# Optimization experiments

Hardware: AMD Instinct MI355X
Metric: run time of the kernel (lower is better)

The kernel has to match this reference:

```python
import jax, jax.numpy as jnp
import numpy as np

NUM_USER = 50000
NUM_ITEM = 40000
N = NUM_USER + NUM_ITEM
E_HALF = 500000
DIM = 64
NUM_ROUTING = 3
NEG_SLOPE = 0.01


def setup_inputs() -> dict:
    key = jax.random.key(0)
    ks = jax.random.split(key, 10)
    rng = np.random.default_rng(0)
    u = rng.integers(0, NUM_USER, E_HALF)
    it = rng.integers(NUM_USER, N, E_HALF)
    edge_index = jnp.asarray(
        np.stack([np.concatenate([u, it]), np.concatenate([it, u])]), dtype=jnp.int64
    )  # [2, 1M] bidirected user-item edges
    return {
        "edge_index": edge_index,
        "v_feat": jax.random.normal(ks[0], (NUM_ITEM, 2048), jnp.float32),
        "t_feat": jax.random.normal(ks[1], (NUM_ITEM, 384), jnp.float32),
        "pref_v": jax.random.normal(ks[2], (NUM_USER, DIM), jnp.float32),
        "pref_t": jax.random.normal(ks[3], (NUM_USER, DIM), jnp.float32),
        "W_v": jax.random.normal(ks[4], (2048, DIM), jnp.float32) * 0.02,
        "b_v": jnp.zeros((DIM,), jnp.float32),
        "W_t": jax.random.normal(ks[5], (384, DIM), jnp.float32) * 0.05,
        "b_t": jnp.zeros((DIM,), jnp.float32),
        "id_embedding": jax.random.normal(ks[6], (N, DIM), jnp.float32),
        "conf": jax.random.normal(ks[7], (N, 2), jnp.float32),
    }


def l2norm(x, eps=1e-12):
    n = jnp.sqrt(jnp.sum(x * x, axis=1, keepdims=True))
    return x / jnp.maximum(n, eps)


def leaky_relu(x):
    return jnp.where(x >= 0, x, NEG_SLOPE * x)


def segment_softmax(logits, seg, n):
    m = jax.ops.segment_max(logits, seg, num_segments=n)
    m = jnp.where(jnp.isfinite(m), m, 0.0)  # empty segments
    e = jnp.exp(logits - jax.lax.stop_gradient(m)[seg])
    s = jax.ops.segment_sum(e, seg, num_segments=n)
    return e / (s[seg] + 1e-16)


def gat_conv(x, ei):
    # dot-product attention, segment softmax over targets, scatter-add
    src, dst = ei[0], ei[1]
    xj = x[src]  # [E, D]
    alpha = jnp.sum(x[dst] * xj, axis=-1)  # [E]
    alpha = segment_softmax(alpha, dst, x.shape[0])
    out = jax.ops.segment_sum(xj * alpha[:, None], dst, num_segments=x.shape[0])
    return out, alpha


def sage_mean(x, ei, w):
    src, dst = ei[0], ei[1]
    msg = x[src] * w  # [E, D]
    s = jax.ops.segment_sum(msg, dst, num_segments=x.shape[0])
    cnt = jax.ops.segment_sum(jnp.ones((ei.shape[1],), x.dtype), dst, num_segments=x.shape[0])
    return s / jnp.maximum(cnt, 1.0)[:, None]


def cgcn(feat, pref, W, b, ei):
    features = l2norm(leaky_relu(feat @ W + b))  # [num_item, D]
    pref = l2norm(pref)
    for _ in range(NUM_ROUTING):
        x = jnp.concatenate([pref, features], axis=0)
        xh, _ = gat_conv(x, ei)
        pref = l2norm(pref + xh[:NUM_USER])
    x = jnp.concatenate([pref, features], axis=0)
    ei2 = jnp.concatenate([ei, ei[::-1]], axis=1)  # add reversed edges
    xh, alpha = gat_conv(x, ei2)
    return x + leaky_relu(xh), alpha[:, None]


def egcn(id_emb, ei, w):
    ei2 = jnp.concatenate([ei, ei[::-1]], axis=1)
    x = l2norm(id_emb)
    h1 = leaky_relu(sage_mean(x, ei2, w))
    h2 = leaky_relu(sage_mean(h1, ei2, w))
    return x + h1 + h2


def reference(edge_index, v_feat, t_feat, pref_v, pref_t, W_v, b_v, W_t, b_t,
              id_embedding, conf):
    v_rep, weight_v = cgcn(v_feat, pref_v, W_v, b_v, edge_index)
    t_rep, weight_t = cgcn(t_feat, pref_t, W_t, b_t, edge_index)
    content_rep = jnp.concatenate([v_rep, t_rep], axis=1)  # [N, 2D]
    weight = jnp.concatenate([weight_v, weight_t], axis=1)  # [2E, 2]
    # weight_mode == 'confid'
    confidence = jnp.concatenate([conf[edge_index[0]], conf[edge_index[1]]], axis=0)
    weight = jnp.max(weight * confidence, axis=1, keepdims=True)
    weight = jax.nn.relu(weight)  # pruning
    id_rep = egcn(id_embedding, edge_index, weight)
    return jnp.concatenate([id_rep, content_rep], axis=1)  # [N, 3D]
```

## Files before the change

kernel.cpp:

```cpp
#include <hip/hip_runtime.h>
#include <hip/hip_bf16.h>
#include <cstdint>
#include <cstddef>

#define NUSER 50000
#define NITEM 40000
#define NNODE 90000
#define NE    1000000
#define DIM   64

typedef __attribute__((ext_vector_type(8))) short short8;
typedef __attribute__((ext_vector_type(4))) float f32x4;

constexpr size_t O_XV   = 0;
constexpr size_t O_XT   = 5760000;
constexpr size_t O_X0   = 11520000;
constexpr size_t O_EV   = 17280000;
constexpr size_t O_ET   = 18280000;
constexpr size_t O_WE   = 19280000;
constexpr size_t O_SV   = 20280000;
constexpr size_t O_STT  = 20370000;
constexpr size_t O_DEG  = 20460000;
constexpr size_t O_RP   = 20550000;
constexpr size_t O_FILL = 20650000;
constexpr size_t O_SRC  = 20750000;
constexpr size_t O_BSUM = 21750000;
constexpr size_t O_BOFF = 21751000;
constexpr size_t O_H1   = 0;
constexpr size_t SW_VHI = 0;
constexpr size_t SW_VLO = 131072;
constexpr size_t SW_THI = 262144;
constexpr size_t SW_TLO = 286720;

__device__ __forceinline__ float leaky(float x) { return x >= 0.f ? x : 0.01f * x; }

__device__ __forceinline__ short f2bf(float x) {
  __hip_bfloat16 h = __float2bfloat16(x);
  return *reinterpret_cast<short*>(&h);
}
__device__ __forceinline__ float bf2f(short s) {
  __hip_bfloat16 h;
  *reinterpret_cast<short*>(&h) = s;
  return __bfloat162float(h);
}

__global__ void deg_count_kernel(const int* __restrict__ ei, int* __restrict__ deg) {
  int e = blockIdx.x * 256 + threadIdx.x;
  if (e >= NE) return;
  atomicAdd(&deg[ei[NE + e]], 1);
}

__global__ void block_sum_kernel(const int* __restrict__ deg, int* __restrict__ bsum) {
  __shared__ int sd[4];
  int i = blockIdx.x * 256 + threadIdx.x;
  int v = (i < NNODE) ? deg[i] : 0;
#pragma unroll
  for (int off = 32; off > 0; off >>= 1) v += __shfl_xor(v, off, 64);
  if ((threadIdx.x & 63) == 0) sd[threadIdx.x >> 6] = v;
  __syncthreads();
  if (threadIdx.x == 0) bsum[blockIdx.x] = sd[0] + sd[1] + sd[2] + sd[3];
}

__global__ void scan_bsum_kernel(const int* __restrict__ bsum, int* __restrict__ boff, int nb) {
  __shared__ int s[512];
  int t = threadIdx.x;
  int v = (t < nb) ? bsum[t] : 0;
  s[t] = v;
  __syncthreads();
  for (int off = 1; off < 512; off <<= 1) {
    int x = (t >= off) ? s[t - off] : 0;
    __syncthreads();
    s[t] += x;
    __syncthreads();
  }
  if (t < nb) boff[t] = s[t] - v;
}

__global__ void scan_final_kernel(const int* __restrict__ deg, const int* __restrict__ boff,
                                  int* __restrict__ row_ptr, int* __restrict__ fill) {
  __shared__ int s[256];
  int t = threadIdx.x;
  int i = blockIdx.x * 256 + t;
  int v = (i < NNODE) ? deg[i] : 0;
  s[t] = v;
  __syncthreads();
  for (int off = 1; off < 256; off <<= 1) {
    int x = (t >= off) ? s[t - off] : 0;
    __syncthreads();
    s[t] += x;
    __syncthreads();
  }
  int incl = s[t];
  int base = boff[blockIdx.x];
  if (i < NNODE) {
    row_ptr[i] = base + incl - v;
    fill[i] = base + incl - v;
    if (i == NNODE - 1) row_ptr[NNODE] = base + incl;
  }
}

__global__ void csr_fill_kernel(const int* __restrict__ ei, int* __restrict__ fill,
                                int* __restrict__ srcs) {
  int e = blockIdx.x * 256 + threadIdx.x;
  if (e >= NE) return;
  int s = ei[e], d = ei[NE + e];
  int slot = atomicAdd(&fill[d], 1);
  srcs[slot] = s;
}

__global__ void wsplit_kernel(const float* __restrict__ W, short* __restrict__ hi,
                              short* __restrict__ lo, int nelem) {
  int t = blockIdx.x * 256 + threadIdx.x;
  if (t >= nelem) return;
  int j = t & 7, sl = (t >> 3) & 15, q = (t >> 7) & 3, nt = (t >> 9) & 3, kt = t >> 11;
  int k = kt * 32 + q * 8 + j, n = nt * 16 + sl;
  float x = W[k * 64 + n];
  short h = f2bf(x);
  hi[t] = h;
  lo[t] = f2bf(x - bf2f(h));
}

__global__ __launch_bounds__(256) void gemm_mfma_kernel(const float* __restrict__ A,
                                                        const short* __restrict__ Whi,
                                                        const short* __restrict__ Wlo,
                                                        const float* __restrict__ bias,
                                                        float* __restrict__ out, int K) {
  __shared__ short Bsh[8192];
  __shared__ short Bsl[8192];
  int tid = threadIdx.x;
  int w = tid >> 6, lane = tid & 63, q = lane >> 4, sl = lane & 15;
  int m0 = blockIdx.x * 64;
  const float* arow = A + (size_t)(m0 + w * 16 + sl) * K;
  f32x4 acc[4] = {{0.f, 0.f, 0.f, 0.f}, {0.f, 0.f, 0.f, 0.f},
                  {0.f, 0.f, 0.f, 0.f}, {0.f, 0.f, 0.f, 0.f}};
  int nchunk = K >> 7;
  for (int c = 0; c < nchunk; ++c) {
    __syncthreads();
    const float4* srch = (const float4*)(Whi + (size_t)c * 8192);
    const float4* srcl = (const float4*)(Wlo + (size_t)c * 8192);
    float4* dsth = (float4*)Bsh;
    float4* dstl = (float4*)Bsl;
#pragma unroll
    for (int r = 0; r < 4; ++r) {
      dsth[r * 256 + tid] = srch[r * 256 + tid];
      dstl[r * 256 + tid] = srcl[r * 256 + tid];
    }
    __syncthreads();
#pragma unroll
    for (int kt = 0; kt < 4; ++kt) {
      int k = c * 128 + kt * 32 + q * 8;
      float4 a0 = *(const float4*)&arow[k];
      float4 a1 = *(const float4*)&arow[k + 4];
      float av[8] = {a0.x, a0.y, a0.z, a0.w, a1.x, a1.y, a1.z, a1.w};
      short8 ah, al;
#pragma unroll
      for (int j = 0; j < 8; ++j) {
        short h = f2bf(av[j]);
        ah[j] = h;
        al[j] = f2bf(av[j] - bf2f(h));
      }
#pragma unroll
      for (int nt = 0; nt < 4; ++nt) {
        short8 bh = *(short8*)&Bsh[(kt * 4 + nt) * 512 + lane * 8];
        short8 bl = *(short8*)&Bsl[(kt * 4 + nt) * 512 + lane * 8];
        acc[nt] = __builtin_amdgcn_mfma_f32_16x16x32_bf16(ah, bh, acc[nt], 0, 0, 0);
        acc[nt] = __builtin_amdgcn_mfma_f32_16x16x32_bf16(ah, bl, acc[nt], 0, 0, 0);
        acc[nt] = __builtin_amdgcn_mfma_f32_16x16x32_bf16(al, bh, acc[nt], 0, 0, 0);
      }
    }
  }
  float bnt[4];
#pragma unroll
  for (int nt = 0; nt < 4; ++nt) bnt[nt] = bias[nt * 16 + sl];
  float v[4][4];
#pragma unroll
  for (int nt = 0; nt < 4; ++nt)
#pragma unroll
    for (int i = 0; i < 4; ++i) v[nt][i] = leaky(acc[nt][i] + bnt[nt]);
#pragma unroll
  for (int i = 0; i < 4; ++i) {
    float ss = v[0][i] * v[0][i] + v[1][i] * v[1][i] + v[2][i] * v[2][i] + v[3][i] * v[3][i];
    ss += __shfl_xor(ss, 1);
    ss += __shfl_xor(ss, 2);
    ss += __shfl_xor(ss, 4);
    ss += __shfl_xor(ss, 8);
    float rinv = 1.f / fmaxf(sqrtf(ss), 1e-12f);
    int row = m0 + w * 16 + q * 4 + i;
#pragma unroll
    for (int nt = 0; nt < 4; ++nt)
      out[(size_t)row * 64 + nt * 16 + sl] = v[nt][i] * rinv;
  }
}

__global__ __launch_bounds__(256) void l2norm_all_kernel(const float* __restrict__ pv,
                                                         const float* __restrict__ pt,
                                                         const float* __restrict__ id,
                                                         float* __restrict__ xv,
                                                         float* __restrict__ xt,
                                                         float* __restrict__ x0) {
  int wid = (blockIdx.x * 256 + threadIdx.x) >> 6;
  int lane = threadIdx.x & 63, sub = lane >> 4, sl = lane & 15;
  int r = wid * 4 + sub;
  if (r >= 2 * NUSER + NNODE) return;
  const float* in;
  float* outp;
  int row;
  if (r < NUSER) { in = pv; outp = xv; row = r; }
  else if (r < 2 * NUSER) { in = pt; outp = xt; row = r - NUSER; }
  else { in = id; outp = x0; row = r - 2 * NUSER; }
  float4 v = *(const float4*)&in[(size_t)row * 64 + sl * 4];
  float ss = v.x * v.x + v.y * v.y + v.z * v.z + v.w * v.w;
  ss += __shfl_xor(ss, 1);
  ss += __shfl_xor(ss, 2);
  ss += __shfl_xor(ss, 4);
  ss += __shfl_xor(ss, 8);
  float rinv = 1.f / fmaxf(sqrtf(ss), 1e-12f);
  v.x *= rinv; v.y *= rinv; v.z *= rinv; v.w *= rinv;
  *(float4*)&outp[(size_t)row * 64 + sl * 4] = v;
}

__global__ __launch_bounds__(256) void routing_kernel(float* __restrict__ xv,
                                                      float* __restrict__ xt,
                                                      const int* __restrict__ rp,
                                                      const int* __restrict__ srcs) {
  int wid = (blockIdx.x * 256 + threadIdx.x) >> 6;
  int lane = threadIdx.x & 63, sub = lane >> 4, sl = lane & 15;
  if (wid >= 2 * NUSER) return;
  float* x = (wid < NUSER) ? xv : xt;
  int row = (wid < NUSER) ? wid : wid - NUSER;
  float4 p = *(const float4*)&x[(size_t)row * 64 + sl * 4];
  int jb = rp[row], je = rp[row + 1];
  float S = 0.f;
  float4 acc = {0.f, 0.f, 0.f, 0.f};
  for (int j0 = jb; j0 < je; j0 += 4) {
    int j = j0 + sub;
    bool valid = j < je;
    int jj = valid ? j : jb;
    int s = srcs[jj];
    float4 f = *(const float4*)&x[(size_t)s * 64 + sl * 4];
    float d = p.x * f.x + p.y * f.y + p.z * f.z + p.w * f.w;
    d += __shfl_xor(d, 1);
    d += __shfl_xor(d, 2);
    d += __shfl_xor(d, 4);
    d += __shfl_xor(d, 8);
    float e = valid ? __expf(d) : 0.f;
    S += e;
    acc.x += e * f.x; acc.y += e * f.y; acc.z += e * f.z; acc.w += e * f.w;
  }
  S += __shfl_xor(S, 16); S += __shfl_xor(S, 32);
  acc.x += __shfl_xor(acc.x, 16); acc.x += __shfl_xor(acc.x, 32);
  acc.y += __shfl_xor(acc.y, 16); acc.y += __shfl_xor(acc.y, 32);
  acc.z += __shfl_xor(acc.z, 16); acc.z += __shfl_xor(acc.z, 32);
  acc.w += __shfl_xor(acc.w, 16); acc.w += __shfl_xor(acc.w, 32);
  if (je > jb) {
    float r = 1.f / S;
    p.x += acc.x * r; p.y += acc.y * r; p.z += acc.z * r; p.w += acc.w * r;
  }
  float ss = p.x * p.x + p.y * p.y + p.z * p.z + p.w * p.w;
  ss += __shfl_xor(ss, 1);
  ss += __shfl_xor(ss, 2);
  ss += __shfl_xor(ss, 4);
  ss += __shfl_xor(ss, 8);
  float rinv = 1.f / fmaxf(sqrtf(ss), 1e-12f);
  if (sub == 0) {
    float4 o = {p.x * rinv, p.y * rinv, p.z * rinv, p.w * rinv};
    *(float4*)&x[(size_t)row * 64 + sl * 4] = o;
  }
}

__global__ __launch_bounds__(256) void gat_final_kernel(const float* __restrict__ xv,
                                                        const float* __restrict__ xt,
                                                        const int* __restrict__ rp,
                                                        const int* __restrict__ srcs,
                                                        float* __restrict__ eV,
                                                        float* __restrict__ eT,
                                                        float* __restrict__ SV,
                                                        float* __restrict__ ST,
                                                        float* __restrict__ out) {
  int wid = (blockIdx.x * 256 + threadIdx.x) >> 6;
  int lane = threadIdx.x & 63, sub = lane >> 4, sl = lane & 15;
  if (wid >= 2 * NNODE) return;
  const float* x;
  float* eOut;
  float* Sout;
  int row, col;
  if (wid < NNODE) { x = xv; eOut = eV; Sout = SV; row = wid; col = 64; }
  else { x = xt; eOut = eT; Sout = ST; row = wid - NNODE; col = 128; }
  float4 xn = *(const float4*)&x[(size_t)row * 64 + sl * 4];
  int jb = rp[row], je = rp[row + 1];
  float S = 0.f;
  float4 acc = {0.f, 0.f, 0.f, 0.f};
  for (int j0 = jb; j0 < je; j0 += 4) {
    int j = j0 + sub;
    bool valid = j < je;
    int jj = valid ? j : jb;
    int s = srcs[jj];
    float4 f = *(const float4*)&x[(size_t)s * 64 + sl * 4];
    float d = xn.x * f.x + xn.y * f.y + xn.z * f.z + xn.w * f.w;
    d += __shfl_xor(d, 1);
    d += __shfl_xor(d, 2);
    d += __shfl_xor(d, 4);
    d += __shfl_xor(d, 8);
    float e = valid ? __expf(d) : 0.f;
    if (valid && sl == 0) eOut[j] = e;
    S += e;
    acc.x += e * f.x; acc.y += e * f.y; acc.z += e * f.z; acc.w += e * f.w;
  }
  S += __shfl_xor(S, 16); S += __shfl_xor(S, 32);
  acc.x += __shfl_xor(acc.x, 16); acc.x += __shfl_xor(acc.x, 32);
  acc.y += __shfl_xor(acc.y, 16); acc.y += __shfl_xor(acc.y, 32);
  acc.z += __shfl_xor(acc.z, 16); acc.z += __shfl_xor(acc.z, 32);
  acc.w += __shfl_xor(acc.w, 16); acc.w += __shfl_xor(acc.w, 32);
  if (lane == 0) Sout[row] = S;
  float4 o;
  if (je > jb) {
    float r = 1.f / S;
    o.x = xn.x + leaky(acc.x * r);
    o.y = xn.y + leaky(acc.y * r);
    o.z = xn.z + leaky(acc.z * r);
    o.w = xn.w + leaky(acc.w * r);
  } else {
    o = xn;
  }
  if (sub == 0) *(float4*)&out[(size_t)row * 192 + col + sl * 4] = o;
}

__global__ __launch_bounds__(256) void egcn_h1_kernel(const float* __restrict__ x0,
                                                      const int* __restrict__ rp,
                                                      const int* __restrict__ srcs,
                                                      const float* __restrict__ eV,
                                                      const float* __restrict__ eT,
                                                      const float* __restrict__ SV,
                                                      const float* __restrict__ ST,
                                                      const float* __restrict__ conf,
                                                      float* __restrict__ wE,
                                                      float* __restrict__ h1) {
  int wid = (blockIdx.x * 256 + threadIdx.x) >> 6;
  int lane = threadIdx.x & 63, sub = lane >> 4, sl = lane & 15;
  if (wid >= NNODE) return;
  int jb = rp[wid], je = rp[wid + 1];
  float rv = 0.f, rt = 0.f;
  if (je > jb) {
    rv = 0.5f / SV[wid];
    rt = 0.5f / ST[wid];
  }
  float4 acc = {0.f, 0.f, 0.f, 0.f};
  for (int j0 = jb; j0 < je; j0 += 4) {
    int j = j0 + sub;
    bool valid = j < je;
    int jj = valid ? j : jb;
    int s = srcs[jj];
    float w = fmaxf(fmaxf(eV[jj] * rv * conf[2 * s], eT[jj] * rt * conf[2 * s + 1]), 0.f);
    if (!valid) w = 0.f;
    if (valid && sl == 0) wE[j] = w;
    float4 f = *(const float4*)&x0[(size_t)s * 64 + sl * 4];
    acc.x += f.x * w; acc.y += f.y * w; acc.z += f.z * w; acc.w += f.w * w;
  }
  acc.x += __shfl_xor(acc.x, 16); acc.x += __shfl_xor(acc.x, 32);
  acc.y += __shfl_xor(acc.y, 16); acc.y += __shfl_xor(acc.y, 32);
  acc.z += __shfl_xor(acc.z, 16); acc.z += __shfl_xor(acc.z, 32);
  acc.w += __shfl_xor(acc.w, 16); acc.w += __shfl_xor(acc.w, 32);
  if (sub == 0) {
    float4 o = {0.f, 0.f, 0.f, 0.f};
    if (je > jb) {
      float r = 1.f / (float)(je - jb);
      o.x = leaky(acc.x * r); o.y = leaky(acc.y * r);
      o.z = leaky(acc.z * r); o.w = leaky(acc.w * r);
    }
    *(float4*)&h1[(size_t)wid * 64 + sl * 4] = o;
  }
}

__global__ __launch_bounds__(256) void egcn_h2_kernel(const float* __restrict__ x0,
                                                      const float* __restrict__ h1,
                                                      const int* __restrict__ rp,
                                                      const int* __restrict__ srcs,
                                                      const float* __restrict__ wE,
                                                      float* __restrict__ out) {
  int wid = (blockIdx.x * 256 + threadIdx.x) >> 6;
  int lane = threadIdx.x & 63, sub = lane >> 4, sl = lane & 15;
  if (wid >= NNODE) return;
  int jb = rp[wid], je = rp[wid + 1];
  float4 acc = {0.f, 0.f, 0.f, 0.f};
  for (int j0 = jb; j0 < je; j0 += 4) {
    int j = j0 + sub;
    bool valid = j < je;
    int jj = valid ? j : jb;
    int s = srcs[jj];
    float w = valid ? wE[jj] : 0.f;
    float4 f = *(const float4*)&h1[(size_t)s * 64 + sl * 4];
    acc.x += f.x * w; acc.y += f.y * w; acc.z += f.z * w; acc.w += f.w * w;
  }
  acc.x += __shfl_xor(acc.x, 16); acc.x += __shfl_xor(acc.x, 32);
  acc.y += __shfl_xor(acc.y, 16); acc.y += __shfl_xor(acc.y, 32);
  acc.z += __shfl_xor(acc.z, 16); acc.z += __shfl_xor(acc.z, 32);
  acc.w += __shfl_xor(acc.w, 16); acc.w += __shfl_xor(acc.w, 32);
  if (sub == 0) {
    float4 h2 = {0.f, 0.f, 0.f, 0.f};
    if (je > jb) {
      float r = 1.f / (float)(je - jb);
      h2.x = leaky(acc.x * r); h2.y = leaky(acc.y * r);
      h2.z = leaky(acc.z * r); h2.w = leaky(acc.w * r);
    }
    float4 a = *(const float4*)&x0[(size_t)wid * 64 + sl * 4];
    float4 b = *(const float4*)&h1[(size_t)wid * 64 + sl * 4];
    float4 o = {a.x + b.x + h2.x, a.y + b.y + h2.y, a.z + b.z + h2.z, a.w + b.w + h2.w};
    *(float4*)&out[(size_t)wid * 192 + sl * 4] = o;
  }
}

extern "C" void kernel_launch(void* const* d_in, const int* in_sizes, int n_in,
                              void* d_out, int out_size, void* d_ws, size_t ws_size,
                              hipStream_t stream) {
  const int* ei = (const int*)d_in[0];
  const float* v_feat = (const float*)d_in[1];
  const float* t_feat = (const float*)d_in[2];
  const float* pref_v = (const float*)d_in[3];
  const float* pref_t = (const float*)d_in[4];
  const float* W_v = (const float*)d_in[5];
  const float* b_v = (const float*)d_in[6];
  const float* W_t = (const float*)d_in[7];
  const float* b_t = (const float*)d_in[8];
  const float* id_emb = (const float*)d_in[9];
  const float* conf = (const float*)d_in[10];
  float* out = (float*)d_out;

  float* ws = (float*)d_ws;
  float* xv = ws + O_XV;
  float* xt = ws + O_XT;
  float* x0 = ws + O_X0;
  float* eV = ws + O_EV;
  float* eT = ws + O_ET;
  float* wE = ws + O_WE;
  float* SV = ws + O_SV;
  float* ST = ws + O_STT;
  int* deg = (int*)(ws + O_DEG);
  int* row_ptr = (int*)(ws + O_RP);
  int* fill = (int*)(ws + O_FILL);
  int* srcs = (int*)(ws + O_SRC);
  int* bsum = (int*)(ws + O_BSUM);
  int* boff = (int*)(ws + O_BOFF);
  float* h1 = ws + O_H1;
  short* wsp = (short*)(ws + O_X0);
  short* WvHi = wsp + SW_VHI;
  short* WvLo = wsp + SW_VLO;
  short* WtHi = wsp + SW_THI;
  short* WtLo = wsp + SW_TLO;

  const int NB = (NNODE + 255) / 256;

  hipMemsetAsync(deg, 0, NNODE * sizeof(int), stream);
  deg_count_kernel<<<(NE + 255) / 256, 256, 0, stream>>>(ei, deg);
  block_sum_kernel<<<NB, 256, 0, stream>>>(deg, bsum);
  scan_bsum_kernel<<<1, 512, 0, stream>>>(bsum, boff, NB);
  scan_final_kernel<<<NB, 256, 0, stream>>>(deg, boff, row_ptr, fill);
  csr_fill_kernel<<<(NE + 255) / 256, 256, 0, stream>>>(ei, fill, srcs);

  wsplit_kernel<<<(2048 * 64 + 255) / 256, 256, 0, stream>>>(W_v, WvHi, WvLo, 2048 * 64);
  wsplit_kernel<<<(384 * 64 + 255) / 256, 256, 0, stream>>>(W_t, WtHi, WtLo, 384 * 64);

  gemm_mfma_kernel<<<NITEM / 64, 256, 0, stream>>>(v_feat, WvHi, WvLo, b_v,
                                                   xv + (size_t)NUSER * 64, 2048);
  gemm_mfma_kernel<<<NITEM / 64, 256, 0, stream>>>(t_feat, WtHi, WtLo, b_t,
                                                   xt + (size_t)NUSER * 64, 384);

  l2norm_all_kernel<<<(2 * NUSER + NNODE) / 16, 256, 0, stream>>>(pref_v, pref_t, id_emb,
                                                                  xv, xt, x0);

  for (int it = 0; it < 3; ++it)
    routing_kernel<<<2 * NUSER / 4, 256, 0, stream>>>(xv, xt, row_ptr, srcs);

  gat_final_kernel<<<2 * NNODE / 4, 256, 0, stream>>>(xv, xt, row_ptr, srcs, eV, eT, SV, ST, out);

  egcn_h1_kernel<<<NNODE / 4, 256, 0, stream>>>(x0, row_ptr, srcs, eV, eT, SV, ST, conf, wE, h1);
  egcn_h2_kernel<<<NNODE / 4, 256, 0, stream>>>(x0, h1, row_ptr, srcs, wE, out);
}
```

Before: 1.058 ms.

## Fuse routing iterations per user with LDS neighbor cache and bf16 gathers

Merges the three routing launches and the user half of the final GAT pass into one per-user kernel. It caches up to 32 neighbor rows in LDS so iterations after the first skip global gathers, and packs v and t features into one interleaved bf16 table so a single gather serves both modalities. Item nodes get their own GAT kernel that reads the routed user rows. The EGCN layers now gather bf16 copies of x0 and h1, and the confidence-weighted edge values are precomputed. This cuts launch count and gather bandwidth at the cost of bf16 rounding in the attention and aggregation inputs.

After: 973.0 us. 1.09x faster.

```diff
diff --git a/kernel.cpp b/kernel.cpp
--- a/kernel.cpp
+++ b/kernel.cpp
@@ -8,25 +8,29 @@
 #define NNODE 90000
 #define NE    1000000
 #define DIM   64
+#define CAP   32
 
 typedef __attribute__((ext_vector_type(8))) short short8;
 typedef __attribute__((ext_vector_type(4))) float f32x4;
 
-constexpr size_t O_XV   = 0;
-constexpr size_t O_XT   = 5760000;
-constexpr size_t O_X0   = 11520000;
-constexpr size_t O_EV   = 17280000;
-constexpr size_t O_ET   = 18280000;
-constexpr size_t O_WE   = 19280000;
-constexpr size_t O_SV   = 20280000;
-constexpr size_t O_STT  = 20370000;
-constexpr size_t O_DEG  = 20460000;
-constexpr size_t O_RP   = 20550000;
-constexpr size_t O_FILL = 20650000;
-constexpr size_t O_SRC  = 20750000;
-constexpr size_t O_BSUM = 21750000;
-constexpr size_t O_BOFF = 21751000;
-constexpr size_t O_H1   = 0;
+constexpr size_t O_XVT  = 0;
+constexpr size_t O_X0   = 5760000;
+constexpr size_t O_X0B  = 11520000;
+constexpr size_t O_H1B  = 14400000;
+constexpr size_t O_XVF  = 17280000;
+constexpr size_t O_XTF  = 19840000;
+constexpr size_t O_AE   = 22400000;
+constexpr size_t O_BE   = 23400000;
+constexpr size_t O_WE   = 24400000;
+constexpr size_t O_SV   = 25400000;
+constexpr size_t O_ST   = 25490000;
+constexpr size_t O_DEG  = 25580000;
+constexpr size_t O_RP   = 25670000;
+constexpr size_t O_FILL = 25770000;
+constexpr size_t O_SRC  = 25870000;
+constexpr size_t O_BSUM = 26870000;
+constexpr size_t O_BOFF = 26871000;
+constexpr size_t O_WSPL = 26880000;
 constexpr size_t SW_VHI = 0;
 constexpr size_t SW_VLO = 131072;
 constexpr size_t SW_THI = 262144;
@@ -34,14 +38,38 @@
 
 __device__ __forceinline__ float leaky(float x) { return x >= 0.f ? x : 0.01f * x; }
 
-__device__ __forceinline__ short f2bf(float x) {
+__device__ __forceinline__ unsigned short f2bfu(float x) {
   __hip_bfloat16 h = __float2bfloat16(x);
-  return *reinterpret_cast<short*>(&h);
-}
+  return *reinterpret_cast<unsigned short*>(&h);
+}
+__device__ __forceinline__ short f2bf(float x) { return (short)f2bfu(x); }
 __device__ __forceinline__ float bf2f(short s) {
-  __hip_bfloat16 h;
-  *reinterpret_cast<short*>(&h) = s;
-  return __bfloat162float(h);
+  unsigned int u = ((unsigned int)(unsigned short)s) << 16;
+  return __uint_as_float(u);
+}
+__device__ __forceinline__ void bf8_to_f32(uint4 u, float* f) {
+  f[0] = __uint_as_float(u.x << 16); f[1] = __uint_as_float(u.x & 0xffff0000u);
+  f[2] = __uint_as_float(u.y << 16); f[3] = __uint_as_float(u.y & 0xffff0000u);
+  f[4] = __uint_as_float(u.z << 16); f[5] = __uint_as_float(u.z & 0xffff0000u);
+  f[6] = __uint_as_float(u.w << 16); f[7] = __uint_as_float(u.w & 0xffff0000u);
+}
+__device__ __forceinline__ uint4 f32_to_bf8(const float* f) {
+  uint4 u;
+  u.x = (uint32_t)f2bfu(f[0]) | ((uint32_t)f2bfu(f[1]) << 16);
+  u.y = (uint32_t)f2bfu(f[2]) | ((uint32_t)f2bfu(f[3]) << 16);
+  u.z = (uint32_t)f2bfu(f[4]) | ((uint32_t)f2bfu(f[5]) << 16);
+  u.w = (uint32_t)f2bfu(f[6]) | ((uint32_t)f2bfu(f[7]) << 16);
+  return u;
+}
+__device__ __forceinline__ void bf4_to_f32(uint2 u, float* f) {
+  f[0] = __uint_as_float(u.x << 16); f[1] = __uint_as_float(u.x & 0xffff0000u);
+  f[2] = __uint_as_float(u.y << 16); f[3] = __uint_as_float(u.y & 0xffff0000u);
+}
+__device__ __forceinline__ uint2 f32_to_bf4(const float* f) {
+  uint2 u;
+  u.x = (uint32_t)f2bfu(f[0]) | ((uint32_t)f2bfu(f[1]) << 16);
+  u.y = (uint32_t)f2bfu(f[2]) | ((uint32_t)f2bfu(f[3]) << 16);
+  return u;
 }
 
 __global__ void deg_count_kernel(const int* __restrict__ ei, int* __restrict__ deg) {
@@ -124,7 +152,9 @@
                                                         const short* __restrict__ Whi,
                                                         const short* __restrict__ Wlo,
                                                         const float* __restrict__ bias,
-                                                        float* __restrict__ out, int K) {
+                                                        float* __restrict__ outF,
+                                                        unsigned short* __restrict__ xvt,
+                                                        int colbase, int K) {
   __shared__ short Bsh[8192];
   __shared__ short Bsl[8192];
   int tid = threadIdx.x;
@@ -187,224 +217,313 @@
     float rinv = 1.f / fmaxf(sqrtf(ss), 1e-12f);
     int row = m0 + w * 16 + q * 4 + i;
 #pragma unroll
-    for (int nt = 0; nt < 4; ++nt)
-      out[(size_t)row * 64 + nt * 16 + sl] = v[nt][i] * rinv;
-  }
-}
-
-__global__ __launch_bounds__(256) void l2norm_all_kernel(const float* __restrict__ pv,
-                                                         const float* __restrict__ pt,
-                                                         const float* __restrict__ id,
-                                                         float* __restrict__ xv,
-                                                         float* __restrict__ xt,
-                                                         float* __restrict__ x0) {
+    for (int nt = 0; nt < 4; ++nt) {
+      float val = v[nt][i] * rinv;
+      outF[(size_t)row * 64 + nt * 16 + sl] = val;
+      xvt[(size_t)(NUSER + row) * 128 + colbase + nt * 16 + sl] = f2bfu(val);
+    }
+  }
+}
+
+__global__ __launch_bounds__(256) void l2norm_id_kernel(const float* __restrict__ id,
+                                                        float* __restrict__ x0,
+                                                        unsigned short* __restrict__ X0b) {
   int wid = (blockIdx.x * 256 + threadIdx.x) >> 6;
   int lane = threadIdx.x & 63, sub = lane >> 4, sl = lane & 15;
   int r = wid * 4 + sub;
-  if (r >= 2 * NUSER + NNODE) return;
-  const float* in;
-  float* outp;
-  int row;
-  if (r < NUSER) { in = pv; outp = xv; row = r; }
-  else if (r < 2 * NUSER) { in = pt; outp = xt; row = r - NUSER; }
-  else { in = id; outp = x0; row = r - 2 * NUSER; }
-  float4 v = *(const float4*)&in[(size_t)row * 64 + sl * 4];
+  if (r >= NNODE) return;
+  float4 v = *(const float4*)&id[(size_t)r * 64 + sl * 4];
   float ss = v.x * v.x + v.y * v.y + v.z * v.z + v.w * v.w;
   ss += __shfl_xor(ss, 1);
   ss += __shfl_xor(ss, 2);
   ss += __shfl_xor(ss, 4);
   ss += __shfl_xor(ss, 8);
   float rinv = 1.f / fmaxf(sqrtf(ss), 1e-12f);
-  v.x *= rinv; v.y *= rinv; v.z *= rinv; v.w *= rinv;
-  *(float4*)&outp[(size_t)row * 64 + sl * 4] = v;
-}
-
-__global__ __launch_bounds__(256) void routing_kernel(float* __restrict__ xv,
-                                                      float* __restrict__ xt,
-                                                      const int* __restrict__ rp,
-                                                      const int* __restrict__ srcs) {
-  int wid = (blockIdx.x * 256 + threadIdx.x) >> 6;
-  int lane = threadIdx.x & 63, sub = lane >> 4, sl = lane & 15;
-  if (wid >= 2 * NUSER) return;
-  float* x = (wid < NUSER) ? xv : xt;
-  int row = (wid < NUSER) ? wid : wid - NUSER;
-  float4 p = *(const float4*)&x[(size_t)row * 64 + sl * 4];
-  int jb = rp[row], je = rp[row + 1];
+  float f[4] = {v.x * rinv, v.y * rinv, v.z * rinv, v.w * rinv};
+  *(float4*)&x0[(size_t)r * 64 + sl * 4] = *(float4*)f;
+  *(uint2*)&X0b[(size_t)r * 64 + sl * 4] = f32_to_bf4(f);
+}
+
+__global__ __launch_bounds__(256) void routing_user_kernel(
+    const float* __restrict__ pref_v, const float* __restrict__ pref_t,
+    unsigned short* __restrict__ XVT,
+    const int* __restrict__ rp, const int* __restrict__ srcs,
+    const float* __restrict__ conf,
+    float* __restrict__ Ae, float* __restrict__ Be,
+    float* __restrict__ SV, float* __restrict__ ST,
+    float* __restrict__ out) {
+  __shared__ unsigned short cache[4][CAP * 128];
+  int wv = threadIdx.x >> 6;
+  int u = blockIdx.x * 4 + wv;
+  if (u >= NUSER) return;
+  int lane = threadIdx.x & 63;
+  int sub = lane >> 4, sl = lane & 15, half = sl >> 3, e8 = sl & 7;
+  unsigned short* myc = cache[wv];
+
+  const float* psrc = half ? pref_t : pref_v;
+  float p[8];
+  *(float4*)&p[0] = *(const float4*)&psrc[(size_t)u * 64 + e8 * 8];
+  *(float4*)&p[4] = *(const float4*)&psrc[(size_t)u * 64 + e8 * 8 + 4];
+  float ss = 0.f;
+#pragma unroll
+  for (int k = 0; k < 8; ++k) ss += p[k] * p[k];
+  ss += __shfl_xor(ss, 1); ss += __shfl_xor(ss, 2); ss += __shfl_xor(ss, 4);
+  float rinv = 1.f / fmaxf(sqrtf(ss), 1e-12f);
+#pragma unroll
+  for (int k = 0; k < 8; ++k) p[k] *= rinv;
+
+  int jb = rp[u], je = rp[u + 1], deg = je - jb;
+
+  for (int it = 0; it < 3; ++it) {
+    float S = 0.f;
+    float acc[8] = {0.f, 0.f, 0.f, 0.f, 0.f, 0.f, 0.f, 0.f};
+    for (int i0 = 0; i0 < deg; i0 += 4) {
+      int i = i0 + sub;
+      bool valid = i < deg;
+      int ii = valid ? i : 0;
+      int j = jb + ii;
+      int s = srcs[j];
+      uint4 u4;
+      if (it == 0) {
+        u4 = *(const uint4*)&XVT[(size_t)s * 128 + sl * 8];
+        if (valid && i < CAP) *(uint4*)&myc[i * 128 + sl * 8] = u4;
+      } else {
+        if (ii < CAP) u4 = *(const uint4*)&myc[ii * 128 + sl * 8];
+        else u4 = *(const uint4*)&XVT[(size_t)s * 128 + sl * 8];
+      }
+      float f[8];
+      bf8_to_f32(u4, f);
+      float d = 0.f;
+#pragma unroll
+      for (int k = 0; k < 8; ++k) d += p[k] * f[k];
+      d += __shfl_xor(d, 1); d += __shfl_xor(d, 2); d += __shfl_xor(d, 4);
+      float e = valid ? __expf(d) : 0.f;
+      S += e;
+#pragma unroll
+      for (int k = 0; k < 8; ++k) acc[k] += e * f[k];
+    }
+    S += __shfl_xor(S, 16); S += __shfl_xor(S, 32);
+#pragma unroll
+    for (int k = 0; k < 8; ++k) {
+      acc[k] += __shfl_xor(acc[k], 16);
+      acc[k] += __shfl_xor(acc[k], 32);
+    }
+    if (deg > 0) {
+      float r = 1.f / S;
+#pragma unroll
+      for (int k = 0; k < 8; ++k) p[k] += acc[k] * r;
+    }
+    ss = 0.f;
+#pragma unroll
+    for (int k = 0; k < 8; ++k) ss += p[k] * p[k];
+    ss += __shfl_xor(ss, 1); ss += __shfl_xor(ss, 2); ss += __shfl_xor(ss, 4);
+    rinv = 1.f / fmaxf(sqrtf(ss), 1e-12f);
+#pragma unroll
+    for (int k = 0; k < 8; ++k) p[k] *= rinv;
+  }
+
   float S = 0.f;
-  float4 acc = {0.f, 0.f, 0.f, 0.f};
-  for (int j0 = jb; j0 < je; j0 += 4) {
-    int j = j0 + sub;
-    bool valid = j < je;
-    int jj = valid ? j : jb;
-    int s = srcs[jj];
-    float4 f = *(const float4*)&x[(size_t)s * 64 + sl * 4];
-    float d = p.x * f.x + p.y * f.y + p.z * f.z + p.w * f.w;
-    d += __shfl_xor(d, 1);
-    d += __shfl_xor(d, 2);
-    d += __shfl_xor(d, 4);
-    d += __shfl_xor(d, 8);
+  float acc[8] = {0.f, 0.f, 0.f, 0.f, 0.f, 0.f, 0.f, 0.f};
+  for (int i0 = 0; i0 < deg; i0 += 4) {
+    int i = i0 + sub;
+    bool valid = i < deg;
+    int ii = valid ? i : 0;
+    int j = jb + ii;
+    int s = srcs[j];
+    uint4 u4;
+    if (ii < CAP) u4 = *(const uint4*)&myc[ii * 128 + sl * 8];
+    else u4 = *(const uint4*)&XVT[(size_t)s * 128 + sl * 8];
+    float f[8];
+    bf8_to_f32(u4, f);
+    float d = 0.f;
+#pragma unroll
+    for (int k = 0; k < 8; ++k) d += p[k] * f[k];
+    d += __shfl_xor(d, 1); d += __shfl_xor(d, 2); d += __shfl_xor(d, 4);
+    float dot_o = __shfl_xor(d, 8);
     float e = valid ? __expf(d) : 0.f;
     S += e;
-    acc.x += e * f.x; acc.y += e * f.y; acc.z += e * f.z; acc.w += e * f.w;
+#pragma unroll
+    for (int k = 0; k < 8; ++k) acc[k] += e * f[k];
+    if (valid && sl == 0) {
+      float2 c = *(const float2*)&conf[2 * s];
+      Ae[j] = e * c.x;
+      Be[j] = __expf(dot_o) * c.y;
+    }
   }
   S += __shfl_xor(S, 16); S += __shfl_xor(S, 32);
-  acc.x += __shfl_xor(acc.x, 16); acc.x += __shfl_xor(acc.x, 32);
-  acc.y += __shfl_xor(acc.y, 16); acc.y += __shfl_xor(acc.y, 32);
-  acc.z += __shfl_xor(acc.z, 16); acc.z += __shfl_xor(acc.z, 32);
-  acc.w += __shfl_xor(acc.w, 16); acc.w += __shfl_xor(acc.w, 32);
-  if (je > jb) {
-    float r = 1.f / S;
-    p.x += acc.x * r; p.y += acc.y * r; p.z += acc.z * r; p.w += acc.w * r;
-  }
-  float ss = p.x * p.x + p.y * p.y + p.z * p.z + p.w * p.w;
-  ss += __shfl_xor(ss, 1);
-  ss += __shfl_xor(ss, 2);
-  ss += __shfl_xor(ss, 4);
-  ss += __shfl_xor(ss, 8);
-  float rinv = 1.f / fmaxf(sqrtf(ss), 1e-12f);
+#pragma unroll
+  for (int k = 0; k < 8; ++k) {
+    acc[k] += __shfl_xor(acc[k], 16);
+    acc[k] += __shfl_xor(acc[k], 32);
+  }
+  float St = __shfl(S, 8);
+  if (lane == 0) { SV[u] = S; ST[u] = St; }
   if (sub == 0) {
-    float4 o = {p.x * rinv, p.y * rinv, p.z * rinv, p.w * rinv};
-    *(float4*)&x[(size_t)row * 64 + sl * 4] = o;
-  }
-}
-
-__global__ __launch_bounds__(256) void gat_final_kernel(const float* __restrict__ xv,
-                                                        const float* __restrict__ xt,
-                                                        const int* __restrict__ rp,
-                                                        const int* __restrict__ srcs,
-                                                        float* __restrict__ eV,
-                                                        float* __restrict__ eT,
-                                                        float* __restrict__ SV,
-                                                        float* __restrict__ ST,
-                                                        float* __restrict__ out) {
+    float o[8];
+    if (deg > 0) {
+      float r = 1.f / S;
+#pragma unroll
+      for (int k = 0; k < 8; ++k) o[k] = p[k] + leaky(acc[k] * r);
+    } else {
+#pragma unroll
+      for (int k = 0; k < 8; ++k) o[k] = p[k];
+    }
+    size_t ob = (size_t)u * 192 + 64 + half * 64 + e8 * 8;
+    *(float4*)&out[ob] = *(float4*)&o[0];
+    *(float4*)&out[ob + 4] = *(float4*)&o[4];
+    *(uint4*)&XVT[(size_t)u * 128 + sl * 8] = f32_to_bf8(p);
+  }
+}
+
+__global__ __launch_bounds__(256) void gat_item_kernel(
+    const unsigned short* __restrict__ XVT,
+    const float* __restrict__ XVf, const float* __restrict__ XTf,
+    const int* __restrict__ rp, const int* __restrict__ srcs,
+    const float* __restrict__ conf,
+    float* __restrict__ Ae, float* __restrict__ Be,
+    float* __restrict__ SV, float* __restrict__ ST,
+    float* __restrict__ out) {
   int wid = (blockIdx.x * 256 + threadIdx.x) >> 6;
+  if (wid >= NITEM) return;
+  int lane = threadIdx.x & 63;
+  int sub = lane >> 4, sl = lane & 15, half = sl >> 3, e8 = sl & 7;
+  int row = NUSER + wid;
+  const float* xsrc = half ? XTf : XVf;
+  float xn[8];
+  *(float4*)&xn[0] = *(const float4*)&xsrc[(size_t)wid * 64 + e8 * 8];
+  *(float4*)&xn[4] = *(const float4*)&xsrc[(size_t)wid * 64 + e8 * 8 + 4];
+  int jb = rp[row], je = rp[row + 1], deg = je - jb;
+  float S = 0.f;
+  float acc[8] = {0.f, 0.f, 0.f, 0.f, 0.f, 0.f, 0.f, 0.f};
+  for (int i0 = 0; i0 < deg; i0 += 4) {
+    int i = i0 + sub;
+    bool valid = i < deg;
+    int j = jb + (valid ? i : 0);
+    int s = srcs[j];
+    uint4 u4 = *(const uint4*)&XVT[(size_t)s * 128 + sl * 8];
+    float f[8];
+    bf8_to_f32(u4, f);
+    float d = 0.f;
+#pragma unroll
+    for (int k = 0; k < 8; ++k) d += xn[k] * f[k];
+    d += __shfl_xor(d, 1); d += __shfl_xor(d, 2); d += __shfl_xor(d, 4);
+    float dot_o = __shfl_xor(d, 8);
+    float e = valid ? __expf(d) : 0.f;
+    S += e;
+#pragma unroll
+    for (int k = 0; k < 8; ++k) acc[k] += e * f[k];
+    if (valid && sl == 0) {
+      float2 c = *(const float2*)&conf[2 * s];
+      Ae[j] = e * c.x;
+      Be[j] = __expf(dot_o) * c.y;
+    }
+  }
+  S += __shfl_xor(S, 16); S += __shfl_xor(S, 32);
+#pragma unroll
+  for (int k = 0; k < 8; ++k) {
+    acc[k] += __shfl_xor(acc[k], 16);
+    acc[k] += __shfl_xor(acc[k], 32);
+  }
+  float St = __shfl(S, 8);
+  if (lane == 0) { SV[row] = S; ST[row] = St; }
+  if (sub == 0) {
+    float o[8];
+    if (deg > 0) {
+      float r = 1.f / S;
+#pragma unroll
+      for (int k = 0; k < 8; ++k) o[k] = xn[k] + leaky(acc[k] * r);
+    } else {
+#pragma unroll
+      for (int k = 0; k < 8; ++k) o[k] = xn[k];
+    }
+    size_t ob = (size_t)row * 192 + 64 + half * 64 + e8 * 8;
+    *(float4*)&out[ob] = *(float4*)&o[0];
+    *(float4*)&out[ob + 4] = *(float4*)&o[4];
+  }
+}
+
+__global__ __launch_bounds__(256) void egcn_h1_kernel(
+    const unsigned short* __restrict__ X0b,
+    const int* __restrict__ rp, const int* __restrict__ srcs,
+    const float* __restrict__ Ae, const float* __restrict__ Be,
+    const float* __restrict__ SV, const float* __restrict__ ST,
+    float* __restrict__ wE, unsigned short* __restrict__ H1b) {
+  int wid = (blockIdx.x * 256 + threadIdx.x) >> 6;
+  if (wid >= NNODE) return;
   int lane = threadIdx.x & 63, sub = lane >> 4, sl = lane & 15;
-  if (wid >= 2 * NNODE) return;
-  const float* x;
-  float* eOut;
-  float* Sout;
-  int row, col;
-  if (wid < NNODE) { x = xv; eOut = eV; Sout = SV; row = wid; col = 64; }
-  else { x = xt; eOut = eT; Sout = ST; row = wid - NNODE; col = 128; }
-  float4 xn = *(const float4*)&x[(size_t)row * 64 + sl * 4];
-  int jb = rp[row], je = rp[row + 1];
-  float S = 0.f;
-  float4 acc = {0.f, 0.f, 0.f, 0.f};
-  for (int j0 = jb; j0 < je; j0 += 4) {
-    int j = j0 + sub;
-    bool valid = j < je;
-    int jj = valid ? j : jb;
-    int s = srcs[jj];
-    float4 f = *(const float4*)&x[(size_t)s * 64 + sl * 4];
-    float d = xn.x * f.x + xn.y * f.y + xn.z * f.z + xn.w * f.w;
-    d += __shfl_xor(d, 1);
-    d += __shfl_xor(d, 2);
-    d += __shfl_xor(d, 4);
-    d += __shfl_xor(d, 8);
-    float e = valid ? __expf(d) : 0.f;
-    if (valid && sl == 0) eOut[j] = e;
-    S += e;
-    acc.x += e * f.x; acc.y += e * f.y; acc.z += e * f.z; acc.w += e * f.w;
-  }
-  S += __shfl_xor(S, 16); S += __shfl_xor(S, 32);
-  acc.x += __shfl_xor(acc.x, 16); acc.x += __shfl_xor(acc.x, 32);
-  acc.y += __shfl_xor(acc.y, 16); acc.y += __shfl_xor(acc.y, 32);
-  acc.z += __shfl_xor(acc.z, 16); acc.z += __shfl_xor(acc.z, 32);
-  acc.w += __shfl_xor(acc.w, 16); acc.w += __shfl_xor(acc.w, 32);
-  if (lane == 0) Sout[row] = S;
-  float4 o;
-  if (je > jb) {
-    float r = 1.f / S;
-    o.x = xn.x + leaky(acc.x * r);
-    o.y = xn.y + leaky(acc.y * r);
-    o.z = xn.z + leaky(acc.z * r);
-    o.w = xn.w + leaky(acc.w * r);
-  } else {
-    o = xn;
-  }
-  if (sub == 0) *(float4*)&out[(size_t)row * 192 + col + sl * 4] = o;
-}
-
-__global__ __launch_bounds__(256) void egcn_h1_kernel(const float* __restrict__ x0,
-                                                      const int* __restrict__ rp,
-                                                      const int* __restrict__ srcs,
-                                                      const float* __restrict__ eV,
-                                                      const float* __restrict__ eT,
-                                                      const float* __restrict__ SV,
-                                                      const float* __restrict__ ST,
-                                                      const float* __restrict__ conf,
-                                                      float* __restrict__ wE,
-                                                      float* __restrict__ h1) {
-  int wid = (blockIdx.x * 256 + threadIdx.x) >> 6;
-  int lane = threadIdx.x & 63, sub = lane >> 4, sl = lane & 15;
-  if (wid >= NNODE) return;
-  int jb = rp[wid], je = rp[wid + 1];
+  int jb = rp[wid], je = rp[wid + 1], deg = je - jb;
   float rv = 0.f, rt = 0.f;
-  if (je > jb) {
-    rv = 0.5f / SV[wid];
-    rt = 0.5f / ST[wid];
-  }
-  float4 acc = {0.f, 0.f, 0.f, 0.f};
-  for (int j0 = jb; j0 < je; j0 += 4) {
-    int j = j0 + sub;
-    bool valid = j < je;
-    int jj = valid ? j : jb;
-    int s = srcs[jj];
-    float w = fmaxf(fmaxf(eV[jj] * rv * conf[2 * s], eT[jj] * rt * conf[2 * s + 1]), 0.f);
+  if (deg > 0) { rv = 0.5f / SV[wid]; rt = 0.5f / ST[wid]; }
+  float acc[4] = {0.f, 0.f, 0.f, 0.f};
+  for (int i0 = 0; i0 < deg; i0 += 4) {
+    int i = i0 + sub;
+    bool valid = i < deg;
+    int j = jb + (valid ? i : 0);
+    int s = srcs[j];
+    float w = fmaxf(fmaxf(rv * Ae[j], rt * Be[j]), 0.f);
     if (!valid) w = 0.f;
     if (valid && sl == 0) wE[j] = w;
-    float4 f = *(const float4*)&x0[(size_t)s * 64 + sl * 4];
-    acc.x += f.x * w; acc.y += f.y * w; acc.z += f.z * w; acc.w += f.w * w;
-  }
-  acc.x += __shfl_xor(acc.x, 16); acc.x += __shfl_xor(acc.x, 32);
-  acc.y += __shfl_xor(acc.y, 16); acc.y += __shfl_xor(acc.y, 32);
-  acc.z += __shfl_xor(acc.z, 16); acc.z += __shfl_xor(acc.z, 32);
-  acc.w += __shfl_xor(acc.w, 16); acc.w += __shfl_xor(acc.w, 32);
+    uint2 u2 = *(const uint2*)&X0b[(size_t)s * 64 + sl * 4];
+    float f[4];
+    bf4_to_f32(u2, f);
+#pragma unroll
+    for (int k = 0; k < 4; ++k) acc[k] += w * f[k];
+  }
+#pragma unroll
+  for (int k = 0; k < 4; ++k) {
+    acc[k] += __shfl_xor(acc[k], 16);
+    acc[k] += __shfl_xor(acc[k], 32);
+  }
   if (sub == 0) {
-    float4 o = {0.f, 0.f, 0.f, 0.f};
-    if (je > jb) {
-      float r = 1.f / (float)(je - jb);
-      o.x = leaky(acc.x * r); o.y = leaky(acc.y * r);
-      o.z = leaky(acc.z * r); o.w = leaky(acc.w * r);
-    }
-    *(float4*)&h1[(size_t)wid * 64 + sl * 4] = o;
-  }
-}
-
-__global__ __launch_bounds__(256) void egcn_h2_kernel(const float* __restrict__ x0,
-                                                      const float* __restrict__ h1,
-                                                      const int* __restrict__ rp,
-                                                      const int* __restrict__ srcs,
-                                                      const float* __restrict__ wE,
-                                                      float* __restrict__ out) {
+    float h[4] = {0.f, 0.f, 0.f, 0.f};
+    if (deg > 0) {
+      float r = 1.f / (float)deg;
+#pragma unroll
+      for (int k = 0; k < 4; ++k) h[k] = leaky(acc[k] * r);
+    }
+    *(uint2*)&H1b[(size_t)wid * 64 + sl * 4] = f32_to_bf4(h);
+  }
+}
+
+__global__ __launch_bounds__(256) void egcn_h2_kernel(
+    const float* __restrict__ x0, const unsigned short* __restrict__ H1b,
+    const int* __restrict__ rp, const int* __restrict__ srcs,
+    const float* __restrict__ wE, float* __restrict__ out) {
   int wid = (blockIdx.x * 256 + threadIdx.x) >> 6;
+  if (wid >= NNODE) return;
   int lane = threadIdx.x & 63, sub = lane >> 4, sl = lane & 15;
-  if (wid >= NNODE) return;
-  int jb = rp[wid], je = rp[wid + 1];
-  float4 acc = {0.f, 0.f, 0.f, 0.f};
-  for (int j0 = jb; j0 < je; j0 += 4) {
-    int j = j0 + sub;
-    bool valid = j < je;
-    int jj = valid ? j : jb;
-    int s = srcs[jj];
-    float w = valid ? wE[jj] : 0.f;
-    float4 f = *(const float4*)&h1[(size_t)s * 64 + sl * 4];
-    acc.x += f.x * w; acc.y += f.y * w; acc.z += f.z * w; acc.w += f.w * w;
-  }
-  acc.x += __shfl_xor(acc.x, 16); acc.x += __shfl_xor(acc.x, 32);
-  acc.y += __shfl_xor(acc.y, 16); acc.y += __shfl_xor(acc.y, 32);
-  acc.z += __shfl_xor(acc.z, 16); acc.z += __shfl_xor(acc.z, 32);
-  acc.w += __shfl_xor(acc.w, 16); acc.w += __shfl_xor(acc.w, 32);
+  int jb = rp[wid], je = rp[wid + 1], deg = je - jb;
+  float acc[4] = {0.f, 0.f, 0.f, 0.f};
+  for (int i0 = 0; i0 < deg; i0 += 4) {
+    int i = i0 + sub;
+    bool valid = i < deg;
+    int j = jb + (valid ? i : 0);
+    int s = srcs[j];
+    float w = valid ? wE[j] : 0.f;
+    uint2 u2 = *(const uint2*)&H1b[(size_t)s * 64 + sl * 4];
+    float f[4];
+    bf4_to_f32(u2, f);
+#pragma unroll
+    for (int k = 0; k < 4; ++k) acc[k] += w * f[k];
+  }
+#pragma unroll
+  for (int k = 0; k < 4; ++k) {
+    acc[k] += __shfl_xor(acc[k], 16);
+    acc[k] += __shfl_xor(acc[k], 32);
+  }
   if (sub == 0) {
-    float4 h2 = {0.f, 0.f, 0.f, 0.f};
-    if (je > jb) {
-      float r = 1.f / (float)(je - jb);
-      h2.x = leaky(acc.x * r); h2.y = leaky(acc.y * r);
-      h2.z = leaky(acc.z * r); h2.w = leaky(acc.w * r);
+    float h2[4] = {0.f, 0.f, 0.f, 0.f};
+    if (deg > 0) {
+      float r = 1.f / (float)deg;
+#pragma unroll
+      for (int k = 0; k < 4; ++k) h2[k] = leaky(acc[k] * r);
     }
     float4 a = *(const float4*)&x0[(size_t)wid * 64 + sl * 4];
-    float4 b = *(const float4*)&h1[(size_t)wid * 64 + sl * 4];
-    float4 o = {a.x + b.x + h2.x, a.y + b.y + h2.y, a.z + b.z + h2.z, a.w + b.w + h2.w};
+    uint2 u2 = *(const uint2*)&H1b[(size_t)wid * 64 + sl * 4];
+    float h1[4];
+    bf4_to_f32(u2, h1);
+    float4 o = {a.x + h1[0] + h2[0], a.y + h1[1] + h2[1],
+                a.z + h1[2] + h2[2], a.w + h1[3] + h2[3]};
     *(float4*)&out[(size_t)wid * 192 + sl * 4] = o;
   }
 }
@@ -426,22 +545,24 @@
   float* out = (float*)d_out;
 
   float* ws = (float*)d_ws;
-  float* xv = ws + O_XV;
-  float* xt = ws + O_XT;
+  unsigned short* XVT = (unsigned short*)(ws + O_XVT);
   float* x0 = ws + O_X0;
-  float* eV = ws + O_EV;
-  float* eT = ws + O_ET;
+  unsigned short* X0b = (unsigned short*)(ws + O_X0B);
+  unsigned short* H1b = (unsigned short*)(ws + O_H1B);
+  float* XVf = ws + O_XVF;
+  float* XTf = ws + O_XTF;
+  float* Ae = ws + O_AE;
+  float* Be = ws + O_BE;
   float* wE = ws + O_WE;
   float* SV = ws + O_SV;
-  float* ST = ws + O_STT;
+  float* ST = ws + O_ST;
   int* deg = (int*)(ws + O_DEG);
   int* row_ptr = (int*)(ws + O_RP);
   int* fill = (int*)(ws + O_FILL);
   int* srcs = (int*)(ws + O_SRC);
   int* bsum = (int*)(ws + O_BSUM);
   int* boff = (int*)(ws + O_BOFF);
-  float* h1 = ws + O_H1;
-  short* wsp = (short*)(ws + O_X0);
+  short* wsp = (short*)(ws + O_WSPL);
   short* WvHi = wsp + SW_VHI;
   short* WvLo = wsp + SW_VLO;
   short* WtHi = wsp + SW_THI;
@@ -459,19 +580,17 @@
   wsplit_kernel<<<(2048 * 64 + 255) / 256, 256, 0, stream>>>(W_v, WvHi, WvLo, 2048 * 64);
   wsplit_kernel<<<(384 * 64 + 255) / 256, 256, 0, stream>>>(W_t, WtHi, WtLo, 384 * 64);
 
-  gemm_mfma_kernel<<<NITEM / 64, 256, 0, stream>>>(v_feat, WvHi, WvLo, b_v,
-                                                   xv + (size_t)NUSER * 64, 2048);
-  gemm_mfma_kernel<<<NITEM / 64, 256, 0, stream>>>(t_feat, WtHi, WtLo, b_t,
-                                                   xt + (size_t)NUSER * 64, 384);
-
-  l2norm_all_kernel<<<(2 * NUSER + NNODE) / 16, 256, 0, stream>>>(pref_v, pref_t, id_emb,
-                                                                  xv, xt, x0);
-
-  for (int it = 0; it < 3; ++it)
-    routing_kernel<<<2 * NUSER / 4, 256, 0, stream>>>(xv, xt, row_ptr, srcs);
-
-  gat_final_kernel<<<2 * NNODE / 4, 256, 0, stream>>>(xv, xt, row_ptr, srcs, eV, eT, SV, ST, out);
-
-  egcn_h1_kernel<<<NNODE / 4, 256, 0, stream>>>(x0, row_ptr, srcs, eV, eT, SV, ST, conf, wE, h1);
-  egcn_h2_kernel<<<NNODE / 4, 256, 0, stream>>>(x0, h1, row_ptr, srcs, wE, out);
-}
+  gemm_mfma_kernel<<<NITEM / 64, 256, 0, stream>>>(v_feat, WvHi, WvLo, b_v, XVf, XVT, 0, 2048);
+  gemm_mfma_kernel<<<NITEM / 64, 256, 0, stream>>>(t_feat, WtHi, WtLo, b_t, XTf, XVT, 64, 384);
+
+  l2norm_id_kernel<<<NNODE / 16, 256, 0, stream>>>(id_emb, x0, X0b);
+
+  routing_user_kernel<<<NUSER / 4, 256, 0, stream>>>(pref_v, pref_t, XVT, row_ptr, srcs, conf,
+                                                     Ae, Be, SV, ST, out);
+
+  gat_item_kernel<<<NITEM / 4, 256, 0, stream>>>(XVT, XVf, XTf, row_ptr, srcs, conf,
+                                                 Ae, Be, SV, ST, out);
+
+  egcn_h1_kernel<<<NNODE / 4, 256, 0, stream>>>(X0b, row_ptr, srcs, Ae, Be, SV, ST, wE, H1b);
+  egcn_h2_kernel<<<NNODE / 4, 256, 0, stream>>>(x0, H1b, row_ptr, srcs, wE, out);
+}
```
